# Performance work log

Hardware: AMD Instinct MI355X
Metric: run time of the kernel (lower is better)

The kernel has to match this reference:

```python
import jax, jax.numpy as jnp
import numpy as np

N, DMAX, IN, HID, OUT = 30000, 16, 128, 256, 64


def setup_inputs() -> dict:
    key = jax.random.key(0)
    ks = jax.random.split(key, 12)
    p = lambda k, shape: jax.random.normal(k, shape, dtype=jnp.float32) * 0.05
    return {
        "feat": jax.random.normal(ks[0], (N, IN), dtype=jnp.float32),
        "nbr_idx": jax.random.randint(ks[1], (N, DMAX), 0, N, dtype=jnp.int32),
        "deg": jax.random.randint(ks[2], (N,), 1, DMAX + 1, dtype=jnp.int32),
        # layer 1: LSTM(in=IN, hidden=IN), fc_self/fc_neigh: IN -> HID
        "Wih1": p(ks[3], (4 * IN, IN)),
        "Whh1": p(ks[4], (4 * IN, IN)),
        "bih1": jnp.zeros((4 * IN,), jnp.float32),
        "bhh1": jnp.zeros((4 * IN,), jnp.float32),
        "Wself1": p(ks[5], (HID, IN)),
        "Wneigh1": p(ks[6], (HID, IN)),
        "b1": jnp.zeros((HID,), jnp.float32),
        # layer 2: LSTM(in=HID, hidden=HID), fc_self/fc_neigh: HID -> OUT
        "Wih2": p(ks[7], (4 * HID, HID)),
        "Whh2": p(ks[8], (4 * HID, HID)),
        "bih2": jnp.zeros((4 * HID,), jnp.float32),
        "bhh2": jnp.zeros((4 * HID,), jnp.float32),
        "Wself2": p(ks[9], (OUT, HID)),
        "Wneigh2": p(ks[10], (OUT, HID)),
        "b2": jnp.zeros((OUT,), jnp.float32),
    }


def _lstm_agg(nbr_feats, deg, Wih, Whh, bih, bhh):
    """LSTM over padded neighbor sequences [N, D, F]; returns final hidden [N, H].
    Matches torch nn.LSTM gate order (i, f, g, o), zero initial state; padded
    steps (t >= deg) leave the state untouched, so result equals the hidden
    state at each node's true sequence length."""
    D = nbr_feats.shape[1]
    H = Whh.shape[1]
    h0 = jnp.zeros((nbr_feats.shape[0], H), nbr_feats.dtype)
    xs = (jnp.swapaxes(nbr_feats, 0, 1), jnp.arange(D))  # ([D,N,F], [D])

    def step(carry, x_t):
        h, c = carry
        x, t = x_t
        gates = x @ Wih.T + bih + h @ Whh.T + bhh  # [N, 4H]
        i, f, g, o = jnp.split(gates, 4, axis=-1)
        c_new = jax.nn.sigmoid(f) * c + jax.nn.sigmoid(i) * jnp.tanh(g)
        h_new = jax.nn.sigmoid(o) * jnp.tanh(c_new)
        valid = (t < deg)[:, None]
        return (jnp.where(valid, h_new, h), jnp.where(valid, c_new, c)), None

    (h, _), _ = jax.lax.scan(step, (h0, h0), xs)
    return h


def _sage_layer(x, nbr_idx, deg, Wih, Whh, bih, bhh, Wself, Wneigh, b):
    nbr = x[nbr_idx]  # gather: [N, DMAX, F]
    m = _lstm_agg(nbr, deg, Wih, Whh, bih, bhh)  # [N, H] (H == F)
    return x @ Wself.T + m @ Wneigh.T + b


def reference(feat, nbr_idx, deg,
              Wih1, Whh1, bih1, bhh1, Wself1, Wneigh1, b1,
              Wih2, Whh2, bih2, bhh2, Wself2, Wneigh2, b2):
    h = jax.nn.relu(_sage_layer(feat, nbr_idx, deg,
                                Wih1, Whh1, bih1, bhh1, Wself1, Wneigh1, b1))
    return _sage_layer(h, nbr_idx, deg,
                       Wih2, Whh2, bih2, bhh2, Wself2, Wneigh2, b2)
```

## Files before the change

### kernel.cpp

```cpp
#include <hip/hip_runtime.h>
#include <hip/hip_bf16.h>
#include <stdint.h>


#define NN 30000
#define DMAXX 16

typedef __bf16 bf16_t;
typedef __bf16 bf16x8 __attribute__((ext_vector_type(8)));
typedef float f32x4 __attribute__((ext_vector_type(4)));
typedef unsigned short u16x4 __attribute__((ext_vector_type(4)));

__device__ __align__(16) bf16_t g_hbuf[(size_t)NN * 256];
__device__ __align__(16) bf16_t g_xg1[(size_t)NN * 512];
__device__ __align__(16) bf16_t g_xg2[(size_t)NN * 1024];
__device__ __align__(16) bf16_t g_wbuf[753664];
__device__ int g_perm[NN];

#define OFF_WIH1 0
#define OFF_WHH1 65536
#define OFF_WSELF1 131072
#define OFF_WNEIGH1 163840
#define OFF_WIH2 196608
#define OFF_WHH2 458752
#define OFF_WSELF2 720896
#define OFF_WNEIGH2 737280
#define W_TOTAL 753664

__global__ __launch_bounds__(256)
void cvt_weights(const float* __restrict__ s0, const float* __restrict__ s1,
                 const float* __restrict__ s2, const float* __restrict__ s3,
                 const float* __restrict__ s4, const float* __restrict__ s5,
                 const float* __restrict__ s6, const float* __restrict__ s7)
{
    int i = (blockIdx.x * 256 + threadIdx.x) * 4;
    if (i >= W_TOTAL) return;
    const float* src; int off;
    if      (i < OFF_WHH1)   { src = s0; off = OFF_WIH1; }
    else if (i < OFF_WSELF1) { src = s1; off = OFF_WHH1; }
    else if (i < OFF_WNEIGH1){ src = s2; off = OFF_WSELF1; }
    else if (i < OFF_WIH2)   { src = s3; off = OFF_WNEIGH1; }
    else if (i < OFF_WHH2)   { src = s4; off = OFF_WIH2; }
    else if (i < OFF_WSELF2) { src = s5; off = OFF_WHH2; }
    else if (i < OFF_WNEIGH2){ src = s6; off = OFF_WSELF2; }
    else                     { src = s7; off = OFF_WNEIGH2; }
    float4 v = *reinterpret_cast<const float4*>(src + (i - off));
    bf16_t o[4] __attribute__((aligned(8)));
    o[0] = (bf16_t)v.x; o[1] = (bf16_t)v.y; o[2] = (bf16_t)v.z; o[3] = (bf16_t)v.w;
    *reinterpret_cast<uint2*>(&g_wbuf[i]) = *reinterpret_cast<const uint2*>(o);
}

__global__ __launch_bounds__(256)
void build_perm(const int* __restrict__ deg, int* __restrict__ perm)
{
    __shared__ int s_base[DMAXX + 1];
    const int tid = threadIdx.x;
    if (tid <= DMAXX) s_base[tid] = 0;
    __syncthreads();
    for (int i = tid; i < NN; i += 256) {
        int d = deg[i]; d = d < 0 ? 0 : (d > DMAXX ? DMAXX : d);
        atomicAdd(&s_base[d], 1);
    }
    __syncthreads();
    if (tid == 0) {
        int acc = 0;
        for (int d = 0; d <= DMAXX; ++d) { int c = s_base[d]; s_base[d] = acc; acc += c; }
    }
    __syncthreads();
    for (int i = tid; i < NN; i += 256) {
        int d = deg[i]; d = d < 0 ? 0 : (d > DMAXX ? DMAXX : d);
        int p = atomicAdd(&s_base[d], 1);
        perm[p] = i;
    }
}

__device__ __forceinline__ float fsig(float x) { return 1.0f / (1.0f + __expf(-x)); }
__device__ __forceinline__ float ftanh(float x) { return 1.0f - 2.0f / (__expf(2.0f * x) + 1.0f); }
__device__ __forceinline__ float bf2f(unsigned short s) {
    union { unsigned u; float f; } v; v.u = ((unsigned)s) << 16; return v.f;
}

template<int F, int LDA, int NT, bool XF32>
__device__ __forceinline__ void stage_tile(bf16_t* dst, const void* src, int row0, int tid)
{
    constexpr int UN = F / 8;
    for (int e = tid; e < 64 * UN; e += NT) {
        int m = e / UN, sub = e - m * UN;
        int row = row0 + m; if (row >= NN) row = NN - 1;
        if constexpr (XF32) {
            const float* p = (const float*)src + (size_t)row * F + sub * 8;
            float4 f0 = reinterpret_cast<const float4*>(p)[0];
            float4 f1 = reinterpret_cast<const float4*>(p)[1];
            bf16_t t[8] __attribute__((aligned(16)));
            t[0]=(bf16_t)f0.x; t[1]=(bf16_t)f0.y; t[2]=(bf16_t)f0.z; t[3]=(bf16_t)f0.w;
            t[4]=(bf16_t)f1.x; t[5]=(bf16_t)f1.y; t[6]=(bf16_t)f1.z; t[7]=(bf16_t)f1.w;
            *reinterpret_cast<uint4*>(&dst[m * LDA + sub * 8]) = *reinterpret_cast<const uint4*>(t);
        } else {
            const bf16_t* p = (const bf16_t*)src + (size_t)row * F + sub * 8;
            *reinterpret_cast<uint4*>(&dst[m * LDA + sub * 8]) = *reinterpret_cast<const uint4*>(p);
        }
    }
}

template<int F, int LDA, int NT, bool XF32>
__device__ __forceinline__ void stage_rows(bf16_t* dst, const void* src, const int* nodes, int tid)
{
    constexpr int UN = F / 8;
    for (int e = tid; e < 64 * UN; e += NT) {
        int m = e / UN, sub = e - m * UN;
        int row = nodes[m];
        if constexpr (XF32) {
            const float* p = (const float*)src + (size_t)row * F + sub * 8;
            float4 f0 = reinterpret_cast<const float4*>(p)[0];
            float4 f1 = reinterpret_cast<const float4*>(p)[1];
            bf16_t t[8] __attribute__((aligned(16)));
            t[0]=(bf16_t)f0.x; t[1]=(bf16_t)f0.y; t[2]=(bf16_t)f0.z; t[3]=(bf16_t)f0.w;
            t[4]=(bf16_t)f1.x; t[5]=(bf16_t)f1.y; t[6]=(bf16_t)f1.z; t[7]=(bf16_t)f1.w;
            *reinterpret_cast<uint4*>(&dst[m * LDA + sub * 8]) = *reinterpret_cast<const uint4*>(t);
        } else {
            const bf16_t* p = (const bf16_t*)src + (size_t)row * F + sub * 8;
            *reinterpret_cast<uint4*>(&dst[m * LDA + sub * 8]) = *reinterpret_cast<const uint4*>(p);
        }
    }
}

template<int F, int G, int NW, bool XF32>
__global__ __launch_bounds__(NW * 64, 2)
void xg_gemm(const void* __restrict__ xsrc_v, const bf16_t* __restrict__ W,
             const float* __restrict__ b0, const float* __restrict__ b1v,
             bf16_t* __restrict__ xg)
{
    constexpr int LDA = F + 8, KK = F / 32, NT = NW * 64;
    constexpr int CPW = G / NW;
    constexpr int CT = CPW / 16;
    static_assert(CPW % 16 == 0 && F % 16 == 0, "");
    const int tid = threadIdx.x, wave = tid >> 6, lane = tid & 63;
    const int q = lane >> 4, m16 = lane & 15;
    const int row0 = blockIdx.x * 64;

    __shared__ __align__(16) bf16_t s_x[64 * LDA];
    stage_tile<F, LDA, NT, XF32>(s_x, xsrc_v, row0, tid);
    __syncthreads();

    #pragma unroll
    for (int ct = 0; ct < CT; ++ct) {
        const int lc0 = wave * CPW + ct * 16;
        const int g = lc0 / F, c0 = lc0 - g * F;
        const float bias = b0[lc0 + m16] + b1v[lc0 + m16];
        f32x4 acc[4];
        #pragma unroll
        for (int rt = 0; rt < 4; ++rt)
            #pragma unroll
            for (int r = 0; r < 4; ++r) acc[rt][r] = bias;
        #pragma unroll
        for (int kk = 0; kk < KK; ++kk) {
            const int ko = kk * 32 + q * 8;
            bf16x8 b = *reinterpret_cast<const bf16x8*>(W + (size_t)(lc0 + m16) * F + ko);
            #pragma unroll
            for (int rt = 0; rt < 4; ++rt) {
                bf16x8 a = *reinterpret_cast<const bf16x8*>(&s_x[(rt * 16 + m16) * LDA + ko]);
                acc[rt] = __builtin_amdgcn_mfma_f32_16x16x32_bf16(a, b, acc[rt], 0, 0, 0);
            }
        }
        #pragma unroll
        for (int rt = 0; rt < 4; ++rt)
            #pragma unroll
            for (int r = 0; r < 4; ++r) {
                int row = row0 + rt * 16 + q * 4 + r;
                if (row < NN)
                    xg[(size_t)row * G + (size_t)(c0 + m16) * 4 + g] = (bf16_t)acc[rt][r];
            }
    }
}

template<int F, int NW, int OUTF, bool RELU, bool XF32, typename OutT>
__global__ __launch_bounds__(NW * 64, 2)
void sage_rec(const void* __restrict__ xself_v,
              const bf16_t* __restrict__ xg,
              const int* __restrict__ nbr_idx, const int* __restrict__ deg,
              const int* __restrict__ perm,
              const bf16_t* __restrict__ Whh,
              const bf16_t* __restrict__ Wself, const bf16_t* __restrict__ Wneigh,
              const float* __restrict__ bout, OutT* __restrict__ outp)
{
    constexpr int M = 64, RT = 4, LDA = F + 8, KK = F / 32, NT = NW * 64;
    constexpr int CPW = F / NW, CT = CPW / 16, G4 = 4 * F;
    static_assert(CPW % 16 == 0, "");
    const int tid = threadIdx.x, wave = tid >> 6, lane = tid & 63;
    const int q = lane >> 4, m16 = lane & 15;
    const int slot0 = blockIdx.x * M;

    __shared__ __align__(16) bf16_t s_h[2][M * LDA];
    __shared__ int s_idx[M * DMAXX];
    __shared__ int s_deg[M];
    __shared__ int s_node[M];
    __shared__ int s_tmax;

    for (int i = tid; i < M; i += NT) {
        int slot = slot0 + i; if (slot >= NN) slot = NN - 1;
        int node = perm[slot];
        s_node[i] = node;
        s_deg[i] = deg[node];
    }
    __syncthreads();
    for (int i = tid; i < M * DMAXX; i += NT) {
        int node = s_node[i >> 4];
        int v = nbr_idx[node * DMAXX + (i & 15)];
        if (v < 0) v = 0; if (v >= NN) v = NN - 1;
        s_idx[i] = v;
    }
    for (int i = tid; i < M * LDA; i += NT) s_h[0][i] = (bf16_t)0.0f;
    if (tid == 0) {
        int mx = 1;
        for (int i = 0; i < M; ++i) { int d = s_deg[i]; mx = d > mx ? d : mx; }
        s_tmax = mx;
    }
    __syncthreads();
    const int tmax = s_tmax;

    int dg[RT][4];
    #pragma unroll
    for (int rt = 0; rt < RT; ++rt)
        #pragma unroll
        for (int r = 0; r < 4; ++r)
            dg[rt][r] = s_deg[rt * 16 + q * 4 + r];

    f32x4 c_[RT][CT];
    #pragma unroll
    for (int rt = 0; rt < RT; ++rt)
        #pragma unroll
        for (int ct = 0; ct < CT; ++ct)
            #pragma unroll
            for (int r = 0; r < 4; ++r) c_[rt][ct][r] = 0.0f;

    #pragma unroll 1
    for (int t = 0; t < tmax; ++t) {
        const bf16_t* cur = s_h[t & 1];
        bf16_t* nxt = s_h[(t + 1) & 1];
        #pragma unroll
        for (int ct = 0; ct < CT; ++ct) {
            u16x4 u[RT][4];
            #pragma unroll
            for (int rt = 0; rt < RT; ++rt)
                #pragma unroll
                for (int r = 0; r < 4; ++r) {
                    int row = s_idx[(rt * 16 + q * 4 + r) * DMAXX + t];
                    u[rt][r] = *reinterpret_cast<const u16x4*>(
                        xg + (size_t)row * G4 + (size_t)(wave * CPW + ct * 16 + m16) * 4);
                }
            f32x4 acc[RT][4];
            #pragma unroll
            for (int rt = 0; rt < RT; ++rt)
                #pragma unroll
                for (int g = 0; g < 4; ++g)
                    #pragma unroll
                    for (int r = 0; r < 4; ++r) acc[rt][g][r] = 0.0f;
            #pragma unroll
            for (int kk = 0; kk < KK; ++kk) {
                const int ko = kk * 32 + q * 8;
                bf16x8 ah[RT];
                #pragma unroll
                for (int rt = 0; rt < RT; ++rt)
                    ah[rt] = *reinterpret_cast<const bf16x8*>(&cur[(rt * 16 + m16) * LDA + ko]);
                #pragma unroll
                for (int g = 0; g < 4; ++g) {
                    bf16x8 bh = *reinterpret_cast<const bf16x8*>(
                        Whh + (size_t)(g * F + wave * CPW + ct * 16 + m16) * F + ko);
                    #pragma unroll
                    for (int rt = 0; rt < RT; ++rt)
                        acc[rt][g] = __builtin_amdgcn_mfma_f32_16x16x32_bf16(ah[rt], bh, acc[rt][g], 0, 0, 0);
                }
            }
            #pragma unroll
            for (int rt = 0; rt < RT; ++rt)
                #pragma unroll
                for (int r = 0; r < 4; ++r) {
                    float iv = fsig (acc[rt][0][r] + bf2f(u[rt][r].x));
                    float fv = fsig (acc[rt][1][r] + bf2f(u[rt][r].y));
                    float gv = ftanh(acc[rt][2][r] + bf2f(u[rt][r].z));
                    float ov = fsig (acc[rt][3][r] + bf2f(u[rt][r].w));
                    float cn = fv * c_[rt][ct][r] + iv * gv;
                    float hv = ov * ftanh(cn);
                    const int pos = (rt * 16 + q * 4 + r) * LDA + wave * CPW + ct * 16 + m16;
                    int d = dg[rt][r];
                    if (t < d) {
                        c_[rt][ct][r] = cn;
                        nxt[pos] = (bf16_t)hv;
                    } else if (t == d) {
                        reinterpret_cast<unsigned short*>(nxt)[pos] =
                            reinterpret_cast<const unsigned short*>(cur)[pos];
                    }
                }
        }
        __syncthreads();
    }

    const int fb = tmax & 1;
    const bf16_t* hfin = s_h[fb];
    bf16_t* hstage = s_h[fb ^ 1];
    stage_rows<F, LDA, NT, XF32>(hstage, xself_v, s_node, tid);
    __syncthreads();

    constexpr int NCT = OUTF / 16;
    constexpr int TILES = NCT * RT;
    constexpr int TPW = TILES / NW;
    static_assert(TILES % NW == 0, "");
    #pragma unroll
    for (int tt = 0; tt < TPW; ++tt) {
        int tile = wave * TPW + tt;
        int ot = tile % NCT, rt = tile / NCT;
        f32x4 o;
        o[0] = 0.f; o[1] = 0.f; o[2] = 0.f; o[3] = 0.f;
        #pragma unroll
        for (int kk = 0; kk < KK; ++kk) {
            const int ko = kk * 32 + q * 8;
            bf16x8 axs = *reinterpret_cast<const bf16x8*>(&hstage[(rt * 16 + m16) * LDA + ko]);
            bf16x8 am  = *reinterpret_cast<const bf16x8*>(&hfin[(rt * 16 + m16) * LDA + ko]);
            bf16x8 bs = *reinterpret_cast<const bf16x8*>(Wself  + (size_t)(ot * 16 + m16) * F + ko);
            bf16x8 bn = *reinterpret_cast<const bf16x8*>(Wneigh + (size_t)(ot * 16 + m16) * F + ko);
            o = __builtin_amdgcn_mfma_f32_16x16x32_bf16(axs, bs, o, 0, 0, 0);
            o = __builtin_amdgcn_mfma_f32_16x16x32_bf16(am,  bn, o, 0, 0, 0);
        }
        int ocol = ot * 16 + m16;
        float bias = bout[ocol];
        #pragma unroll
        for (int r = 0; r < 4; ++r) {
            int node = s_node[rt * 16 + q * 4 + r];
            float v = o[r] + bias;
            if (RELU) v = fmaxf(v, 0.0f);
            outp[(size_t)node * OUTF + ocol] = (OutT)v;
        }
    }
}

extern "C" void kernel_launch(void* const* d_in, const int* in_sizes, int n_in,
                              void* d_out, int out_size, void* d_ws, size_t ws_size,
                              hipStream_t stream)
{
    const float* feat    = (const float*)d_in[0];
    const int*   nbr     = (const int*)d_in[1];
    const int*   degp    = (const int*)d_in[2];
    const float* Wih1    = (const float*)d_in[3];
    const float* Whh1    = (const float*)d_in[4];
    const float* bih1    = (const float*)d_in[5];
    const float* bhh1    = (const float*)d_in[6];
    const float* Wself1  = (const float*)d_in[7];
    const float* Wneigh1 = (const float*)d_in[8];
    const float* b1      = (const float*)d_in[9];
    const float* Wih2    = (const float*)d_in[10];
    const float* Whh2    = (const float*)d_in[11];
    const float* bih2    = (const float*)d_in[12];
    const float* bhh2    = (const float*)d_in[13];
    const float* Wself2  = (const float*)d_in[14];
    const float* Wneigh2 = (const float*)d_in[15];
    const float* b2      = (const float*)d_in[16];

    bf16_t *hglob, *wglob, *xg1, *xg2;
    int *permg;
    hipGetSymbolAddress((void**)&hglob, HIP_SYMBOL(g_hbuf));
    hipGetSymbolAddress((void**)&wglob, HIP_SYMBOL(g_wbuf));
    hipGetSymbolAddress((void**)&xg1,   HIP_SYMBOL(g_xg1));
    hipGetSymbolAddress((void**)&xg2,   HIP_SYMBOL(g_xg2));
    hipGetSymbolAddress((void**)&permg, HIP_SYMBOL(g_perm));

    cvt_weights<<<W_TOTAL / 4 / 256, 256, 0, stream>>>(
        Wih1, Whh1, Wself1, Wneigh1, Wih2, Whh2, Wself2, Wneigh2);

    build_perm<<<1, 256, 0, stream>>>(degp, permg);

    const int grid = (NN + 63) / 64;

    xg_gemm<128, 512, 8, true><<<grid, 512, 0, stream>>>(
        feat, wglob + OFF_WIH1, bih1, bhh1, xg1);

    sage_rec<128, 8, 256, true, true, bf16_t><<<grid, 512, 0, stream>>>(
        feat, xg1, nbr, degp, permg, wglob + OFF_WHH1,
        wglob + OFF_WSELF1, wglob + OFF_WNEIGH1, b1, hglob);

    xg_gemm<256, 1024, 8, false><<<grid, 512, 0, stream>>>(
        hglob, wglob + OFF_WIH2, bih2, bhh2, xg2);

    sage_rec<256, 8, 64, false, false, float><<<grid, 512, 0, stream>>>(
        hglob, xg2, nbr, degp, permg, wglob + OFF_WHH2,
        wglob + OFF_WSELF2, wglob + OFF_WNEIGH2, b2, (float*)d_out);
}
```

Measured before the change: 1.243 ms.

## Split recurrent waves over rows, prefetch next-step gate inputs, schedule longest nodes first

The recurrent kernel now runs 16 waves arranged as a column-by-row grid, so each wave handles fewer rows and columns. The precomputed input-gate values for step t+1 are loaded from global memory during step t, so gather latency overlaps the MFMA work instead of stalling each step. The degree permutation is reversed so blocks of high-degree nodes are scheduled first, which reduces the tail. The larger blocks and the tighter launch bound (four blocks of 1024 threads) cap VGPRs per thread. That risks register spills, especially since the prefetch buffers stay live across the whole loop.

After: 1.710 ms. 37.5% more time.

```diff
diff --git a/kernel.cpp b/kernel.cpp
--- a/kernel.cpp
+++ b/kernel.cpp
@@ -64,7 +64,7 @@
     __syncthreads();
     if (tid == 0) {
         int acc = 0;
-        for (int d = 0; d <= DMAXX; ++d) { int c = s_base[d]; s_base[d] = acc; acc += c; }
+        for (int d = DMAXX; d >= 0; --d) { int c = s_base[d]; s_base[d] = acc; acc += c; }
     }
     __syncthreads();
     for (int i = tid; i < NN; i += 256) {
@@ -173,8 +173,8 @@
     }
 }
 
-template<int F, int NW, int OUTF, bool RELU, bool XF32, typename OutT>
-__global__ __launch_bounds__(NW * 64, 2)
+template<int F, int NWC, int NWR, int OUTF, bool RELU, bool XF32, typename OutT>
+__global__ __launch_bounds__(NWC * NWR * 64, 4)
 void sage_rec(const void* __restrict__ xself_v,
               const bf16_t* __restrict__ xg,
               const int* __restrict__ nbr_idx, const int* __restrict__ deg,
@@ -183,11 +183,16 @@
               const bf16_t* __restrict__ Wself, const bf16_t* __restrict__ Wneigh,
               const float* __restrict__ bout, OutT* __restrict__ outp)
 {
-    constexpr int M = 64, RT = 4, LDA = F + 8, KK = F / 32, NT = NW * 64;
-    constexpr int CPW = F / NW, CT = CPW / 16, G4 = 4 * F;
-    static_assert(CPW % 16 == 0, "");
+    constexpr int M = 64, LDA = F + 8, KK = F / 32;
+    constexpr int NW = NWC * NWR, NT = NW * 64;
+    constexpr int RT = M / (16 * NWR);
+    constexpr int CPW = F / NWC, CT = CPW / 16;
+    constexpr int G4 = 4 * F;
+    static_assert(CPW % 16 == 0 && M % (16 * NWR) == 0, "");
     const int tid = threadIdx.x, wave = tid >> 6, lane = tid & 63;
     const int q = lane >> 4, m16 = lane & 15;
+    const int wc = wave % NWC, wr = wave / NWC;
+    const int ROWB = wr * (RT * 16);
     const int slot0 = blockIdx.x * M;
 
     __shared__ __align__(16) bf16_t s_h[2][M * LDA];
@@ -223,7 +228,7 @@
     for (int rt = 0; rt < RT; ++rt)
         #pragma unroll
         for (int r = 0; r < 4; ++r)
-            dg[rt][r] = s_deg[rt * 16 + q * 4 + r];
+            dg[rt][r] = s_deg[ROWB + rt * 16 + q * 4 + r];
 
     f32x4 c_[RT][CT];
     #pragma unroll
@@ -232,6 +237,18 @@
         for (int ct = 0; ct < CT; ++ct)
             #pragma unroll
             for (int r = 0; r < 4; ++r) c_[rt][ct][r] = 0.0f;
+
+    u16x4 u[CT][RT][4];
+    #pragma unroll
+    for (int ct = 0; ct < CT; ++ct)
+        #pragma unroll
+        for (int rt = 0; rt < RT; ++rt)
+            #pragma unroll
+            for (int r = 0; r < 4; ++r) {
+                int row = s_idx[(ROWB + rt * 16 + q * 4 + r) * DMAXX];
+                u[ct][rt][r] = *reinterpret_cast<const u16x4*>(
+                    xg + (size_t)row * G4 + (size_t)(wc * CPW + ct * 16 + m16) * 4);
+            }
 
     #pragma unroll 1
     for (int t = 0; t < tmax; ++t) {
@@ -239,15 +256,6 @@
         bf16_t* nxt = s_h[(t + 1) & 1];
         #pragma unroll
         for (int ct = 0; ct < CT; ++ct) {
-            u16x4 u[RT][4];
-            #pragma unroll
-            for (int rt = 0; rt < RT; ++rt)
-                #pragma unroll
-                for (int r = 0; r < 4; ++r) {
-                    int row = s_idx[(rt * 16 + q * 4 + r) * DMAXX + t];
-                    u[rt][r] = *reinterpret_cast<const u16x4*>(
-                        xg + (size_t)row * G4 + (size_t)(wave * CPW + ct * 16 + m16) * 4);
-                }
             f32x4 acc[RT][4];
             #pragma unroll
             for (int rt = 0; rt < RT; ++rt)
@@ -261,11 +269,11 @@
                 bf16x8 ah[RT];
                 #pragma unroll
                 for (int rt = 0; rt < RT; ++rt)
-                    ah[rt] = *reinterpret_cast<const bf16x8*>(&cur[(rt * 16 + m16) * LDA + ko]);
+                    ah[rt] = *reinterpret_cast<const bf16x8*>(&cur[(ROWB + rt * 16 + m16) * LDA + ko]);
                 #pragma unroll
                 for (int g = 0; g < 4; ++g) {
                     bf16x8 bh = *reinterpret_cast<const bf16x8*>(
-                        Whh + (size_t)(g * F + wave * CPW + ct * 16 + m16) * F + ko);
+                        Whh + (size_t)(g * F + wc * CPW + ct * 16 + m16) * F + ko);
                     #pragma unroll
                     for (int rt = 0; rt < RT; ++rt)
                         acc[rt][g] = __builtin_amdgcn_mfma_f32_16x16x32_bf16(ah[rt], bh, acc[rt][g], 0, 0, 0);
@@ -275,13 +283,13 @@
             for (int rt = 0; rt < RT; ++rt)
                 #pragma unroll
                 for (int r = 0; r < 4; ++r) {
-                    float iv = fsig (acc[rt][0][r] + bf2f(u[rt][r].x));
-                    float fv = fsig (acc[rt][1][r] + bf2f(u[rt][r].y));
-                    float gv = ftanh(acc[rt][2][r] + bf2f(u[rt][r].z));
-                    float ov = fsig (acc[rt][3][r] + bf2f(u[rt][r].w));
+                    float iv = fsig (acc[rt][0][r] + bf2f(u[ct][rt][r].x));
+                    float fv = fsig (acc[rt][1][r] + bf2f(u[ct][rt][r].y));
+                    float gv = ftanh(acc[rt][2][r] + bf2f(u[ct][rt][r].z));
+                    float ov = fsig (acc[rt][3][r] + bf2f(u[ct][rt][r].w));
                     float cn = fv * c_[rt][ct][r] + iv * gv;
                     float hv = ov * ftanh(cn);
-                    const int pos = (rt * 16 + q * 4 + r) * LDA + wave * CPW + ct * 16 + m16;
+                    const int pos = (ROWB + rt * 16 + q * 4 + r) * LDA + wc * CPW + ct * 16 + m16;
                     int d = dg[rt][r];
                     if (t < d) {
                         c_[rt][ct][r] = cn;
@@ -291,6 +299,16 @@
                             reinterpret_cast<const unsigned short*>(cur)[pos];
                     }
                 }
+            if (t + 1 < tmax) {
+                #pragma unroll
+                for (int rt = 0; rt < RT; ++rt)
+                    #pragma unroll
+                    for (int r = 0; r < 4; ++r) {
+                        int row = s_idx[(ROWB + rt * 16 + q * 4 + r) * DMAXX + t + 1];
+                        u[ct][rt][r] = *reinterpret_cast<const u16x4*>(
+                            xg + (size_t)row * G4 + (size_t)(wc * CPW + ct * 16 + m16) * 4);
+                    }
+            }
         }
         __syncthreads();
     }
@@ -302,7 +320,7 @@
     __syncthreads();
 
     constexpr int NCT = OUTF / 16;
-    constexpr int TILES = NCT * RT;
+    constexpr int TILES = NCT * 4;
     constexpr int TPW = TILES / NW;
     static_assert(TILES % NW == 0, "");
     #pragma unroll
@@ -373,14 +391,14 @@
     xg_gemm<128, 512, 8, true><<<grid, 512, 0, stream>>>(
         feat, wglob + OFF_WIH1, bih1, bhh1, xg1);
 
-    sage_rec<128, 8, 256, true, true, bf16_t><<<grid, 512, 0, stream>>>(
+    sage_rec<128, 8, 2, 256, true, true, bf16_t><<<grid, 1024, 0, stream>>>(
         feat, xg1, nbr, degp, permg, wglob + OFF_WHH1,
         wglob + OFF_WSELF1, wglob + OFF_WNEIGH1, b1, hglob);
 
     xg_gemm<256, 1024, 8, false><<<grid, 512, 0, stream>>>(
         hglob, wglob + OFF_WIH2, bih2, bhh2, xg2);
 
-    sage_rec<256, 8, 64, false, false, float><<<grid, 512, 0, stream>>>(
+    sage_rec<256, 8, 2, 64, false, false, float><<<grid, 1024, 0, stream>>>(
         hglob, xg2, nbr, degp, permg, wglob + OFF_WHH2,
         wglob + OFF_WSELF2, wglob + OFF_WNEIGH2, b2, (float*)d_out);
 }
```
